# Performance work log

Measured on AMD Instinct MI355X. Metric: run time of the kernel, lower is better.

## Reference

```python
import jax, jax.numpy as jnp
import numpy as np

N = 50000        # num nodes
E = 1600000      # num edges (avg degree 32)
DIN = 128        # dim_in
DOUT = 256       # dim_out
DA = 32          # dim_atten
SLOPE = 0.2      # leaky_relu negative slope


def setup_inputs() -> dict:
    key = jax.random.key(0)
    ks = jax.random.split(key, 9)
    x = jax.random.normal(ks[0], (N, DIN), dtype=jnp.float32)
    row = jax.random.randint(ks[1], (E,), 0, N, dtype=jnp.int32)
    col = jax.random.randint(ks[2], (E,), 0, N, dtype=jnp.int32)
    adj_val = jax.random.uniform(ks[3], (E,), dtype=jnp.float32)
    # learned params (Linear weights stored as [in, out] for x @ W)
    W_row = (jax.random.normal(ks[4], (DIN, DA)) / np.sqrt(DIN)).astype(jnp.float32)
    W_col = (jax.random.normal(ks[5], (DIN, DA)) / np.sqrt(DIN)).astype(jnp.float32)
    W_x = (jax.random.normal(ks[6], (DIN, DOUT)) / np.sqrt(DIN)).astype(jnp.float32)
    b_x = jnp.zeros((DOUT,), dtype=jnp.float32)
    return {"x": x, "row": row, "col": col, "adj_val": adj_val,
            "W_row": W_row, "W_col": W_col, "W_x": W_x, "b_x": b_x}


def reference(x, row, col, adj_val, W_row, W_col, W_x, b_x):
    # per-node attention projections
    a_row = x @ W_row                      # [N, DA]
    a_col = x @ W_col                      # [N, DA]
    # 'Multiply' attention: per-edge dot product scaled by rsqrt(DA)
    atten = jnp.sum(a_row[row] * a_col[col], axis=1) * jax.lax.rsqrt(jnp.float32(DA))  # [E]
    atten = jnp.where(atten >= 0, atten, SLOPE * atten)   # leaky_relu
    atten = jnp.exp(atten - jnp.max(atten))               # global-max-shifted exp
    # row-sum normalization (segment softmax denominator)
    deg = jax.ops.segment_sum(atten, row, num_segments=N)  # [N]
    atten = atten * (1.0 / (deg + 1e-15))[row]             # [E]
    # atten_combine == 'plus': average with original adjacency values
    vals = (adj_val + atten) * 0.5                         # [E]
    # sparse-dense matmul: out[i] = sum_{e: row[e]==i} vals[e] * x[col[e]]
    out = jax.ops.segment_sum(vals[:, None] * x[col], row, num_segments=N)  # [N, DIN]
    return out @ W_x + b_x                                 # [N, DOUT]
```

## Files before the change

### kernel.cpp

```cpp
#include <hip/hip_runtime.h>


#define DIN   128
#define DOUT  256
#define DA    32
#define SLOPE 0.2f
#define RSQRT_DA 0.17677669529663687f
#define BSH   6
#define BCAP  2560
#define CSTRIDE 32
#define NBMAX 800
#define PB_CHUNK 16384

typedef unsigned int uint;
typedef unsigned short ushort;
typedef __attribute__((ext_vector_type(8))) short bf16x8;
typedef __attribute__((ext_vector_type(4))) float f32x4;

static __device__ __forceinline__ ushort f2bf(float f) {
  const uint u = __float_as_uint(f);
  return (ushort)((u + 0x7fffu + ((u >> 16) & 1u)) >> 16);
}

__global__ __launch_bounds__(256) void wconv_kernel(
    const float* __restrict__ Wx, ushort* __restrict__ wxt,
    const float* __restrict__ Wr, const float* __restrict__ Wc,
    ushort* __restrict__ wrct, int* __restrict__ bcursor, int nb) {
  __shared__ ushort s[16][DIN];
  const int t = threadIdx.x;
  const int b = blockIdx.x;
  if (b < 16) {
    const int c0 = b * 16;
#pragma unroll
    for (int u = 0; u < 8; ++u) {
      const int k = u * 16 + (t >> 4);
      s[t & 15][k] = f2bf(Wx[(size_t)k * DOUT + c0 + (t & 15)]);
    }
    __syncthreads();
    const int c = t >> 4;
    const int kk = (t & 15) * 8;
    *(uint4*)(wxt + (size_t)(c0 + c) * DIN + kk) = *(const uint4*)&s[c][kk];
  } else if (b < 20) {
    const int c = (b - 16) * 16 + (t >> 4);
    const int k0 = (t & 15) * 8;
    const float* src = (c < DA) ? (Wr + c) : (Wc + (c - DA));
    ushort h[8];
#pragma unroll
    for (int j = 0; j < 8; ++j) h[j] = f2bf(src[(size_t)(k0 + j) * DA]);
    uint4 v;
    v.x = (uint)h[0] | ((uint)h[1] << 16);
    v.y = (uint)h[2] | ((uint)h[3] << 16);
    v.z = (uint)h[4] | ((uint)h[5] << 16);
    v.w = (uint)h[6] | ((uint)h[7] << 16);
    *(uint4*)(wrct + (size_t)c * DIN + k0) = v;
  } else {
    for (int i = t; i < nb; i += 256) bcursor[i * CSTRIDE] = i * BCAP;
  }
}

__global__ __launch_bounds__(512) void super_kernel(
    const float* __restrict__ x, const ushort* __restrict__ wrct,
    float* __restrict__ a_row, ushort* __restrict__ a_colh,
    ushort* __restrict__ xh,
    const int* __restrict__ row, const int* __restrict__ col,
    const float* __restrict__ adj, int* __restrict__ bcursor,
    int2* __restrict__ ibuf, int nb, int E, int npart, int n) {
  __shared__ union {
    struct { int hist[NBMAX]; int base[NBMAX]; } p;
    ushort xb[32][136];
  } sh;
  const int t = threadIdx.x;

  if ((int)blockIdx.x < npart) {
    int* hist = sh.p.hist;
    int* base = sh.p.base;
    const int e0 = blockIdx.x * PB_CHUNK;
    for (int b = t; b < nb; b += 512) hist[b] = 0;
    __syncthreads();
    for (int u = 0; u < PB_CHUNK / 512; ++u) {
      const int e = e0 + u * 512 + t;
      if (e < E) atomicAdd(&hist[row[e] >> BSH], 1);
    }
    __syncthreads();
    for (int b = t; b < nb; b += 512) {
      const int c = hist[b];
      base[b] = c ? atomicAdd(&bcursor[b * CSTRIDE], c) : 0;
      hist[b] = 0;
    }
    __syncthreads();
    for (int u = 0; u < PB_CHUNK / 512; ++u) {
      const int e = e0 + u * 512 + t;
      if (e < E) {
        const int r = row[e];
        const int b = r >> BSH;
        const int pos = base[b] + atomicAdd(&hist[b], 1);
        ibuf[pos] = make_int2(((r & 63) << 16) | col[e], __float_as_int(adj[e]));
      }
    }
    return;
  }

  const int pb = blockIdx.x - npart;
  const int node0 = pb * 32;
  const float4* xg = (const float4*)(x + (size_t)node0 * DIN);
  if (node0 + 32 <= n) {
#pragma unroll
    for (int u = 0; u < 2; ++u) {
      const int f = t + u * 512;
      const float4 v = xg[f];
      ushort4 h;
      h.x = f2bf(v.x); h.y = f2bf(v.y); h.z = f2bf(v.z); h.w = f2bf(v.w);
      *(ushort4*)&sh.xb[f >> 5][(f & 31) * 4] = h;
      ((ushort4*)(xh + (size_t)node0 * DIN))[f] = h;
    }
  } else {
#pragma unroll
    for (int u = 0; u < 2; ++u) {
      const int f = t + u * 512;
      const int nd = node0 + (f >> 5);
      float4 v;
      if (nd < n) v = xg[f];
      else { v.x = 0.f; v.y = 0.f; v.z = 0.f; v.w = 0.f; }
      ushort4 h;
      h.x = f2bf(v.x); h.y = f2bf(v.y); h.z = f2bf(v.z); h.w = f2bf(v.w);
      *(ushort4*)&sh.xb[f >> 5][(f & 31) * 4] = h;
      if (nd < n) ((ushort4*)(xh + (size_t)node0 * DIN))[f] = h;
    }
  }
  __syncthreads();

  const int w = t >> 6;
  const int l = t & 63;
  const int lr = l & 15;
  const int lk = (l >> 4) * 8;
  const int h2 = w & 1;
  const int q = w >> 1;
  f32x4 acc = {0.f, 0.f, 0.f, 0.f};
#pragma unroll
  for (int kk = 0; kk < 4; ++kk) {
    const bf16x8 a = *(const bf16x8*)&sh.xb[h2 * 16 + lr][kk * 32 + lk];
    const bf16x8 bb =
        *(const bf16x8*)(wrct + (size_t)(q * 16 + lr) * DIN + kk * 32 + lk);
    acc = __builtin_amdgcn_mfma_f32_16x16x32_bf16(a, bb, acc, 0, 0, 0);
  }
  const int colq = q * 16 + lr;
  const int r0 = (l >> 4) * 4;
#pragma unroll
  for (int r = 0; r < 4; ++r) {
    const int node = node0 + h2 * 16 + r0 + r;
    if (node < n) {
      if (colq < DA)
        a_row[(size_t)node * DA + colq] = acc[r] * RSQRT_DA;
      else
        a_colh[(size_t)node * DA + (colq - DA)] = f2bf(acc[r]);
    }
  }
}

#define NODE_BODY(J)                                                    \
  {                                                                     \
    const int2 e = spk[w][half][(J)];                                   \
    const float pv = sp[w][half][(J)];                                  \
    const uint2 xv = xh2[(size_t)e.x * 32 + la];                        \
    const float av = __int_as_float(e.y);                               \
    const float f0 = __uint_as_float(xv.x << 16);                       \
    const float f1 = __uint_as_float(xv.x & 0xffff0000u);               \
    const float f2 = __uint_as_float(xv.y << 16);                       \
    const float f3 = __uint_as_float(xv.y & 0xffff0000u);               \
    aa0 += av * f0; aa1 += av * f1; aa2 += av * f2; aa3 += av * f3;     \
    ap0 += pv * f0; ap1 += pv * f1; ap2 += pv * f2; ap3 += pv * f3;     \
    deg += pv;                                                          \
  }

__global__ __launch_bounds__(512) void node_kernel(
    const uint* __restrict__ xh, const float* __restrict__ a_row,
    const ushort* __restrict__ a_colh, const int* __restrict__ bcursor,
    const int2* __restrict__ ibuf, const ushort* __restrict__ wxt,
    const float* __restrict__ bx, float* __restrict__ out, int n) {
  __shared__ int2  eL[BCAP];
  __shared__ int   cnt[64];
  __shared__ int   excl[65];
  __shared__ int2  spk[8][2][32];
  __shared__ float sp[8][2][32];
  __shared__ float s_ar[8][2][32];
  __shared__ ushort sfeat[64][136];
  const int t = threadIdx.x;
  const int b = blockIdx.x;
  const int node0 = b << BSH;
  const int estart = b * BCAP;
  const int ecnt = bcursor[b * CSTRIDE] - estart;

  if (t < 64) cnt[t] = 0;
  __syncthreads();
  int2 myv[BCAP / 512];
#pragma unroll
  for (int u = 0; u < BCAP / 512; ++u) {
    const int e = u * 512 + t;
    if (e < ecnt) {
      myv[u] = ibuf[estart + e];
      atomicAdd(&cnt[myv[u].x >> 16], 1);
    }
  }
  __syncthreads();
  if (t < 64) {
    const int v = cnt[t];
    int inc = v;
#pragma unroll
    for (int ofs = 1; ofs < 64; ofs <<= 1) {
      const int o = __shfl_up(inc, ofs, 64);
      if (t >= ofs) inc += o;
    }
    excl[t] = inc - v;
    if (t == 63) excl[64] = inc;
    cnt[t] = 0;
  }
  __syncthreads();
#pragma unroll
  for (int u = 0; u < BCAP / 512; ++u) {
    const int e = u * 512 + t;
    if (e < ecnt) {
      const int rl = myv[u].x >> 16;
      const int pos = excl[rl] + atomicAdd(&cnt[rl], 1);
      eL[pos] = make_int2(myv[u].x & 0xffff, myv[u].y);
    }
  }
  __syncthreads();

  const int w = t >> 6;
  const int lane = t & 63;
  const int half = lane >> 5;
  const int la = lane & 31;
  const uint2* xh2 = (const uint2*)xh;

  for (int pp = 0; pp < 4; ++pp) {
    const int rl0 = (pp * 8 + w) * 2;
    const int i = node0 + rl0 + half;
    const int o0 = excl[rl0];
    const int o1 = excl[rl0 + 1];
    const int o2 = excl[rl0 + 2];
    const int d0 = o1 - o0, d1 = o2 - o1;
    const int myoff = half ? o1 : o0;
    const int myd = half ? d1 : d0;
    const int dmax = max(d0, d1);
    s_ar[w][half][la] = (i < n) ? a_row[(size_t)i * DA + la] : 0.f;

    float aa0 = 0.f, aa1 = 0.f, aa2 = 0.f, aa3 = 0.f;
    float ap0 = 0.f, ap1 = 0.f, ap2 = 0.f, ap3 = 0.f;
    float deg = 0.f;

    for (int base = 0; base < dmax; base += 32) {
      const int m = myd - base;
      if (la < m) {
        const int2 e = eL[myoff + base + la];
        spk[w][half][la] = e;
        const uint4* ac = (const uint4*)(a_colh + (size_t)e.x * DA);
        const float* ar = s_ar[w][half];
        float dot = 0.f;
#pragma unroll
        for (int k = 0; k < 4; ++k) {
          const uint4 q = ac[k];
          const float* a = ar + k * 8;
          dot += __uint_as_float(q.x << 16) * a[0] +
                 __uint_as_float(q.x & 0xffff0000u) * a[1] +
                 __uint_as_float(q.y << 16) * a[2] +
                 __uint_as_float(q.y & 0xffff0000u) * a[3] +
                 __uint_as_float(q.z << 16) * a[4] +
                 __uint_as_float(q.z & 0xffff0000u) * a[5] +
                 __uint_as_float(q.w << 16) * a[6] +
                 __uint_as_float(q.w & 0xffff0000u) * a[7];
        }
        const float lg = (dot >= 0.f) ? dot : SLOPE * dot;
        sp[w][half][la] = __expf(lg);
      } else {
        spk[w][half][la] = make_int2(0, 0);
        sp[w][half][la] = 0.f;
      }
      const int mmax = min(32, dmax - base);
      int j = 0;
      for (; j + 8 <= mmax; j += 8) {
#pragma unroll
        for (int u = 0; u < 8; ++u) NODE_BODY(j + u)
      }
      for (; j < mmax; ++j) NODE_BODY(j)
    }
    {
      const float inv = 0.5f / (deg + 1e-15f);
      ushort4 h;
      h.x = f2bf(0.5f * aa0 + inv * ap0);
      h.y = f2bf(0.5f * aa1 + inv * ap1);
      h.z = f2bf(0.5f * aa2 + inv * ap2);
      h.w = f2bf(0.5f * aa3 + inv * ap3);
      *(ushort4*)&sfeat[rl0 + half][la * 4] = h;
    }
  }
  __syncthreads();

  const int lr = lane & 15;
  const int lk = (lane >> 4) * 8;
  const int rt = (w & 3) * 16;
  const int ct0 = (w >> 2) * 128;
  f32x4 acc2[8];
#pragma unroll
  for (int ct = 0; ct < 8; ++ct) acc2[ct] = f32x4{0.f, 0.f, 0.f, 0.f};
#pragma unroll
  for (int kk = 0; kk < 4; ++kk) {
    const bf16x8 a = *(const bf16x8*)&sfeat[rt + lr][kk * 32 + lk];
#pragma unroll
    for (int ct = 0; ct < 8; ++ct) {
      const bf16x8 bb =
          *(const bf16x8*)(wxt + (size_t)(ct0 + ct * 16 + lr) * DIN + kk * 32 + lk);
      acc2[ct] = __builtin_amdgcn_mfma_f32_16x16x32_bf16(a, bb, acc2[ct], 0, 0, 0);
    }
  }
  const int r0e = (lane >> 4) * 4;
#pragma unroll
  for (int ct = 0; ct < 8; ++ct) {
    const int c = ct0 + ct * 16 + lr;
    const float bv = bx[c];
#pragma unroll
    for (int r = 0; r < 4; ++r) {
      const int node = node0 + rt + r0e + r;
      if (node < n) out[(size_t)node * DOUT + c] = acc2[ct][r] + bv;
    }
  }
}

extern "C" void kernel_launch(void* const* d_in, const int* in_sizes, int n_in,
                              void* d_out, int out_size, void* d_ws, size_t ws_size,
                              hipStream_t stream) {
  const float* x   = (const float*)d_in[0];
  const int*   row = (const int*)d_in[1];
  const int*   col = (const int*)d_in[2];
  const float* adj = (const float*)d_in[3];
  const float* Wr  = (const float*)d_in[4];
  const float* Wc  = (const float*)d_in[5];
  const float* Wx  = (const float*)d_in[6];
  const float* bx  = (const float*)d_in[7];
  float* out = (float*)d_out;

  const int n = in_sizes[0] / DIN;
  const int E = in_sizes[1];
  const int nb = (n + 63) >> BSH;
  const int npart = (E + PB_CHUNK - 1) / PB_CHUNK;
  const int nproj = (n + 31) / 32;

  int* w4 = (int*)d_ws;
  float* a_row   = (float*)w4;  w4 += (size_t)n * DA;
  ushort* a_colh = (ushort*)w4; w4 += (size_t)n * DA / 2;
  uint*   xh     = (uint*)w4;   w4 += (size_t)n * DIN / 2;
  int2*   ibuf   = (int2*)w4;   w4 += (size_t)nb * BCAP * 2;
  int*    bcursor= w4;          w4 += (size_t)nb * CSTRIDE;
  ushort* wxt    = (ushort*)w4; w4 += (size_t)DOUT * DIN / 2;
  ushort* wrct   = (ushort*)w4;

  wconv_kernel<<<21, 256, 0, stream>>>(Wx, wxt, Wr, Wc, wrct, bcursor, nb);
  super_kernel<<<npart + nproj, 512, 0, stream>>>(
      x, wrct, a_row, a_colh, (ushort*)xh, row, col, adj, bcursor, ibuf,
      nb, E, npart, n);
  node_kernel<<<nb, 512, 0, stream>>>(
      (const uint*)xh, a_row, a_colh, bcursor, ibuf, wxt, bx, out, n);
}
```

Before: 272.1 us.

## Split node aggregation from output GEMM and halve node bucket size

Buckets now hold 32 nodes instead of 64, which doubles the number of node blocks and cuts per-block LDS (edge list capacity 1408). The fused MFMA projection is taken out of node_kernel: aggregated features are written to a bf16 workspace buffer, and a separate gemm_kernel computes out = feat @ W_x + b. This is meant to raise occupancy and parallelism in the aggregation phase. The cost is an extra global round trip of the N×128 bf16 features, one more launch, and a tighter bucket capacity that could overflow on skewed degree distributions.

```diff
diff --git a/kernel.cpp b/kernel.cpp
--- a/kernel.cpp
+++ b/kernel.cpp
@@ -6,11 +6,12 @@
 #define DA    32
 #define SLOPE 0.2f
 #define RSQRT_DA 0.17677669529663687f
-#define BSH   6
-#define BCAP  2560
+#define BSH   5
+#define BCAP  1408
 #define CSTRIDE 32
-#define NBMAX 800
-#define PB_CHUNK 16384
+#define NBMAX 1600
+#define PB_CHUNK 8192
+#define NU    3
 
 typedef unsigned int uint;
 typedef unsigned short ushort;
@@ -94,7 +95,7 @@
         const int r = row[e];
         const int b = r >> BSH;
         const int pos = base[b] + atomicAdd(&hist[b], 1);
-        ibuf[pos] = make_int2(((r & 63) << 16) | col[e], __float_as_int(adj[e]));
+        ibuf[pos] = make_int2(((r & 31) << 16) | col[e], __float_as_int(adj[e]));
       }
     }
     return;
@@ -175,26 +176,24 @@
 __global__ __launch_bounds__(512) void node_kernel(
     const uint* __restrict__ xh, const float* __restrict__ a_row,
     const ushort* __restrict__ a_colh, const int* __restrict__ bcursor,
-    const int2* __restrict__ ibuf, const ushort* __restrict__ wxt,
-    const float* __restrict__ bx, float* __restrict__ out, int n) {
+    const int2* __restrict__ ibuf, ushort* __restrict__ feath, int n) {
   __shared__ int2  eL[BCAP];
-  __shared__ int   cnt[64];
-  __shared__ int   excl[65];
+  __shared__ int   cnt[32];
+  __shared__ int   excl[33];
   __shared__ int2  spk[8][2][32];
   __shared__ float sp[8][2][32];
   __shared__ float s_ar[8][2][32];
-  __shared__ ushort sfeat[64][136];
   const int t = threadIdx.x;
   const int b = blockIdx.x;
   const int node0 = b << BSH;
   const int estart = b * BCAP;
   const int ecnt = bcursor[b * CSTRIDE] - estart;
 
-  if (t < 64) cnt[t] = 0;
-  __syncthreads();
-  int2 myv[BCAP / 512];
-#pragma unroll
-  for (int u = 0; u < BCAP / 512; ++u) {
+  if (t < 32) cnt[t] = 0;
+  __syncthreads();
+  int2 myv[NU];
+#pragma unroll
+  for (int u = 0; u < NU; ++u) {
     const int e = u * 512 + t;
     if (e < ecnt) {
       myv[u] = ibuf[estart + e];
@@ -202,21 +201,21 @@
     }
   }
   __syncthreads();
-  if (t < 64) {
+  if (t < 32) {
     const int v = cnt[t];
     int inc = v;
 #pragma unroll
-    for (int ofs = 1; ofs < 64; ofs <<= 1) {
-      const int o = __shfl_up(inc, ofs, 64);
+    for (int ofs = 1; ofs < 32; ofs <<= 1) {
+      const int o = __shfl_up(inc, ofs, 32);
       if (t >= ofs) inc += o;
     }
     excl[t] = inc - v;
-    if (t == 63) excl[64] = inc;
+    if (t == 31) excl[32] = inc;
     cnt[t] = 0;
   }
   __syncthreads();
 #pragma unroll
-  for (int u = 0; u < BCAP / 512; ++u) {
+  for (int u = 0; u < NU; ++u) {
     const int e = u * 512 + t;
     if (e < ecnt) {
       const int rl = myv[u].x >> 16;
@@ -232,7 +231,7 @@
   const int la = lane & 31;
   const uint2* xh2 = (const uint2*)xh;
 
-  for (int pp = 0; pp < 4; ++pp) {
+  for (int pp = 0; pp < 2; ++pp) {
     const int rl0 = (pp * 8 + w) * 2;
     const int i = node0 + rl0 + half;
     const int o0 = excl[rl0];
@@ -283,45 +282,50 @@
       }
       for (; j < mmax; ++j) NODE_BODY(j)
     }
-    {
+    if (i < n) {
       const float inv = 0.5f / (deg + 1e-15f);
       ushort4 h;
       h.x = f2bf(0.5f * aa0 + inv * ap0);
       h.y = f2bf(0.5f * aa1 + inv * ap1);
       h.z = f2bf(0.5f * aa2 + inv * ap2);
       h.w = f2bf(0.5f * aa3 + inv * ap3);
-      *(ushort4*)&sfeat[rl0 + half][la * 4] = h;
-    }
-  }
-  __syncthreads();
-
-  const int lr = lane & 15;
-  const int lk = (lane >> 4) * 8;
-  const int rt = (w & 3) * 16;
-  const int ct0 = (w >> 2) * 128;
-  f32x4 acc2[8];
-#pragma unroll
-  for (int ct = 0; ct < 8; ++ct) acc2[ct] = f32x4{0.f, 0.f, 0.f, 0.f};
+      *(ushort4*)(feath + (size_t)i * DIN + la * 4) = h;
+    }
+  }
+}
+
+__global__ __launch_bounds__(256) void gemm_kernel(
+    const ushort* __restrict__ feath, const ushort* __restrict__ wxt,
+    const float* __restrict__ bx, float* __restrict__ out) {
+  const int t = threadIdx.x;
+  const int w = t >> 6;
+  const int l = t & 63;
+  const int row0 = blockIdx.x * 16;
+  const int lr = l & 15;
+  const int lk = (l >> 4) * 8;
+  const int col0 = w * 64;
+
+  f32x4 acc[4] = {f32x4{0.f, 0.f, 0.f, 0.f}, f32x4{0.f, 0.f, 0.f, 0.f},
+                  f32x4{0.f, 0.f, 0.f, 0.f}, f32x4{0.f, 0.f, 0.f, 0.f}};
+  const ushort* Abase = feath + (size_t)(row0 + lr) * DIN + lk;
 #pragma unroll
   for (int kk = 0; kk < 4; ++kk) {
-    const bf16x8 a = *(const bf16x8*)&sfeat[rt + lr][kk * 32 + lk];
-#pragma unroll
-    for (int ct = 0; ct < 8; ++ct) {
-      const bf16x8 bb =
-          *(const bf16x8*)(wxt + (size_t)(ct0 + ct * 16 + lr) * DIN + kk * 32 + lk);
-      acc2[ct] = __builtin_amdgcn_mfma_f32_16x16x32_bf16(a, bb, acc2[ct], 0, 0, 0);
-    }
-  }
-  const int r0e = (lane >> 4) * 4;
-#pragma unroll
-  for (int ct = 0; ct < 8; ++ct) {
-    const int c = ct0 + ct * 16 + lr;
+    const bf16x8 a = *(const bf16x8*)(Abase + kk * 32);
+#pragma unroll
+    for (int ct = 0; ct < 4; ++ct) {
+      const bf16x8 b =
+          *(const bf16x8*)(wxt + (size_t)(col0 + ct * 16 + lr) * DIN + kk * 32 + lk);
+      acc[ct] = __builtin_amdgcn_mfma_f32_16x16x32_bf16(a, b, acc[ct], 0, 0, 0);
+    }
+  }
+  const int crow0 = row0 + (l >> 4) * 4;
+#pragma unroll
+  for (int ct = 0; ct < 4; ++ct) {
+    const int c = col0 + ct * 16 + lr;
     const float bv = bx[c];
 #pragma unroll
-    for (int r = 0; r < 4; ++r) {
-      const int node = node0 + rt + r0e + r;
-      if (node < n) out[(size_t)node * DOUT + c] = acc2[ct][r] + bv;
-    }
+    for (int r = 0; r < 4; ++r)
+      out[(size_t)(crow0 + r) * DOUT + c] = acc[ct][r] + bv;
   }
 }
 
@@ -340,12 +344,13 @@
 
   const int n = in_sizes[0] / DIN;
   const int E = in_sizes[1];
-  const int nb = (n + 63) >> BSH;
+  const int nb = (n + 31) >> BSH;
   const int npart = (E + PB_CHUNK - 1) / PB_CHUNK;
   const int nproj = (n + 31) / 32;
 
   int* w4 = (int*)d_ws;
   float* a_row   = (float*)w4;  w4 += (size_t)n * DA;
+  ushort* feath  = (ushort*)w4; w4 += (size_t)n * DIN / 2;
   ushort* a_colh = (ushort*)w4; w4 += (size_t)n * DA / 2;
   uint*   xh     = (uint*)w4;   w4 += (size_t)n * DIN / 2;
   int2*   ibuf   = (int2*)w4;   w4 += (size_t)nb * BCAP * 2;
@@ -358,5 +363,6 @@
       x, wrct, a_row, a_colh, (ushort*)xh, row, col, adj, bcursor, ibuf,
       nb, E, npart, n);
   node_kernel<<<nb, 512, 0, stream>>>(
-      (const uint*)xh, a_row, a_colh, bcursor, ibuf, wxt, bx, out, n);
-}
+      (const uint*)xh, a_row, a_colh, bcursor, ibuf, feath, n);
+  gemm_kernel<<<n / 16, 256, 0, stream>>>(feath, wxt, bx, out);
+}
```

Result: no change. 268.6 us (-1.3%).
